# Kernel tuning notes

Measured on AMD Instinct MI355X. Metric: run time of the kernel, lower is better.

## Reference

```python
import jax, jax.numpy as jnp
import numpy as np

D_MODEL = 1024
HEADS = 16
D_KEY = D_MODEL // HEADS


def setup_inputs() -> dict:
    key = jax.random.key(0)
    ks = jax.random.split(key, 7)
    B, S = 4, 2048
    queries = jax.random.normal(ks[0], (B, S, D_MODEL), dtype=jnp.float32)
    keys = jax.random.normal(ks[1], (B, S, D_MODEL), dtype=jnp.float32)
    values = jax.random.normal(ks[2], (B, S, D_MODEL), dtype=jnp.float32)
    scale = 1.0 / np.sqrt(D_MODEL)
    # Per-head projection weights, torch Linear layout [out=d_key, in=d_model], stacked over heads
    Wq = jax.random.uniform(ks[3], (HEADS, D_KEY, D_MODEL), jnp.float32, -scale, scale)
    Wk = jax.random.uniform(ks[4], (HEADS, D_KEY, D_MODEL), jnp.float32, -scale, scale)
    Wv = jax.random.uniform(ks[5], (HEADS, D_KEY, D_MODEL), jnp.float32, -scale, scale)
    Wo = jax.random.uniform(ks[6], (D_MODEL, D_MODEL), jnp.float32, -scale, scale)
    return {"queries": queries, "keys": keys, "values": values,
            "Wq": Wq, "Wk": Wk, "Wv": Wv, "Wo": Wo}


def reference(queries, keys, values, Wq, Wk, Wv, Wo):
    # Project per head: [B,S,D] x [H,K,D] -> [B,H,S,K]
    q = jnp.einsum('bsd,hkd->bhsk', queries, Wq)
    k = jnp.einsum('bsd,hkd->bhsk', keys, Wk)
    v = jnp.einsum('bsd,hkd->bhsk', values, Wv)
    attn = jnp.einsum('bhqk,bhsk->bhqs', q, k) / jnp.sqrt(jnp.float32(D_KEY))
    attn = jax.nn.softmax(attn, axis=-1)
    out = jnp.einsum('bhqs,bhsk->bhqk', attn, v)  # [B,H,S,K]
    B, H, S, K = out.shape
    # concat heads along last dim (head order = torch cat order)
    out = out.transpose(0, 2, 1, 3).reshape(B, S, H * K)
    return out @ Wo.T
```

## Files before the change

kernel.cpp:

```cpp
#include <hip/hip_runtime.h>
#include <hip/hip_bf16.h>

typedef __attribute__((ext_vector_type(8))) short short8;
typedef __attribute__((ext_vector_type(4))) short short4v;
typedef __attribute__((ext_vector_type(4))) float f32x4;
typedef __bf16 bf16x8 __attribute__((ext_vector_type(8)));
typedef __attribute__((ext_vector_type(2))) unsigned int u32x2;
typedef __attribute__((ext_vector_type(4))) unsigned int u32x4;

#define DEVI static __device__ __forceinline__

DEVI short f2bs(float f) {
    union { __hip_bfloat16 h; short s; } u;
    u.h = __float2bfloat16(f);
    return u.s;
}

DEVI unsigned pack2(float a, float b) {
    union { short s[2]; unsigned u; } u;
    u.s[0] = f2bs(a);
    u.s[1] = f2bs(b);
    return u.u;
}

DEVI void xchg(unsigned& x, unsigned& y) {
#if __has_builtin(__builtin_amdgcn_permlane32_swap) && __has_builtin(__builtin_amdgcn_permlane16_swap)
    u32x2 t = __builtin_amdgcn_permlane32_swap(x, y, false, false);
    u32x2 r = __builtin_amdgcn_permlane16_swap(t[0], t[1], false, false);
    x = r[0];
    y = r[1];
#else
    asm("v_permlane32_swap_b32 %0, %1" : "+v"(x), "+v"(y));
    asm("v_permlane16_swap_b32 %0, %1" : "+v"(x), "+v"(y));
#endif
}

DEVI f32x4 mfma16(short8 a, short8 b, f32x4 c) {
    return __builtin_amdgcn_mfma_f32_16x16x32_bf16(
        __builtin_bit_cast(bf16x8, a), __builtin_bit_cast(bf16x8, b), c, 0, 0, 0);
}

DEVI void glds16(const short* g, short* l) {
    __builtin_amdgcn_global_load_lds((const __attribute__((address_space(1))) void*)g,
                                     (__attribute__((address_space(3))) void*)l, 16, 0, 0);
}

__global__ __launch_bounds__(256) void cvt_all(const float4* __restrict__ q,
                                               const float4* __restrict__ k,
                                               const float4* __restrict__ v,
                                               const float4* __restrict__ wq,
                                               const float4* __restrict__ wk,
                                               const float4* __restrict__ wv,
                                               const float4* __restrict__ wo,
                                               short4v* __restrict__ dq,
                                               short4v* __restrict__ dk,
                                               short4v* __restrict__ dv,
                                               short4v* __restrict__ dwq,
                                               short4v* __restrict__ dwk,
                                               short4v* __restrict__ dwv,
                                               short4v* __restrict__ dwo) {
    int bid = blockIdx.x;
    float4 x;
    short4v s;
    if (bid < 8192) {
        int i = bid * 256 + threadIdx.x;
        x = q[i]; s.x = f2bs(x.x); s.y = f2bs(x.y); s.z = f2bs(x.z); s.w = f2bs(x.w); dq[i] = s;
        x = k[i]; s.x = f2bs(x.x); s.y = f2bs(x.y); s.z = f2bs(x.z); s.w = f2bs(x.w); dk[i] = s;
        x = v[i]; s.x = f2bs(x.x); s.y = f2bs(x.y); s.z = f2bs(x.z); s.w = f2bs(x.w); dv[i] = s;
    } else {
        int i = (bid - 8192) * 256 + threadIdx.x;
        x = wq[i]; s.x = f2bs(x.x); s.y = f2bs(x.y); s.z = f2bs(x.z); s.w = f2bs(x.w); dwq[i] = s;
        x = wk[i]; s.x = f2bs(x.x); s.y = f2bs(x.y); s.z = f2bs(x.z); s.w = f2bs(x.w); dwk[i] = s;
        x = wv[i]; s.x = f2bs(x.x); s.y = f2bs(x.y); s.z = f2bs(x.z); s.w = f2bs(x.w); dwv[i] = s;
        x = wo[i]; s.x = f2bs(x.x); s.y = f2bs(x.y); s.z = f2bs(x.z); s.w = f2bs(x.w); dwo[i] = s;
    }
}

template <typename EpiT>
DEVI void gemm_body(const short* A, const short* Bw, short* smem, int m0, int n0, EpiT epi) {
    short* As = smem;
    short* Bs = smem + 8192;
    const int t = threadIdx.x;
    const int lane = t & 63, w = t >> 6;
    const int col = lane & 15, quad = lane >> 4;
    const int wm = (w & 1) * 64, wn = (w >> 1) * 64;

    f32x4 acc[4][4];
#pragma unroll
    for (int i = 0; i < 4; ++i)
#pragma unroll
        for (int j = 0; j < 4; ++j) acc[i][j] = (f32x4){0.f, 0.f, 0.f, 0.f};

    for (int kt = 0; kt < 16; ++kt) {
        const int k0 = kt * 64;
#pragma unroll
        for (int j = 0; j < 4; ++j) {
            int cbase = (j * 4 + w) * 64;
            int c = cbase + lane;
            int row = c >> 3, kc = (c & 7) ^ (row & 7);
            glds16(A + (size_t)(m0 + row) * 1024 + k0 + kc * 8, As + cbase * 8);
        }
#pragma unroll
        for (int j = 0; j < 4; ++j) {
            int cbase = (j * 4 + w) * 64;
            int c = cbase + lane;
            int row = c >> 3, kc = (c & 7) ^ (row & 7);
            glds16(Bw + (size_t)(n0 + row) * 1024 + k0 + kc * 8, Bs + cbase * 8);
        }
        __syncthreads();
#pragma unroll
        for (int ks = 0; ks < 2; ++ks) {
            short8 a[4], b[4];
#pragma unroll
            for (int i = 0; i < 4; ++i) {
                int row = wm + i * 16 + col;
                int kc = (ks * 4 + quad) ^ (col & 7);
                a[i] = *(const short8*)(As + (row * 8 + kc) * 8);
            }
#pragma unroll
            for (int i = 0; i < 4; ++i) {
                int row = wn + i * 16 + col;
                int kc = (ks * 4 + quad) ^ (col & 7);
                b[i] = *(const short8*)(Bs + (row * 8 + kc) * 8);
            }
#pragma unroll
            for (int mi = 0; mi < 4; ++mi)
#pragma unroll
                for (int ni = 0; ni < 4; ++ni)
                    acc[mi][ni] = mfma16(a[mi], b[ni], acc[mi][ni]);
        }
        __syncthreads();
    }
    epi(acc, wm, wn, col, quad);
}

__global__ __launch_bounds__(256) void qkv_gemm(const short* __restrict__ xq,
                                                const short* __restrict__ xk,
                                                const short* __restrict__ xv,
                                                const short* __restrict__ wq,
                                                const short* __restrict__ wk,
                                                const short* __restrict__ wv,
                                                short* __restrict__ qp,
                                                short* __restrict__ kp,
                                                short* __restrict__ vpt, float qscale) {
    __shared__ __align__(16) short smem[17408];
    const int z = blockIdx.z;
    const int m0 = blockIdx.y * 128, n0 = blockIdx.x * 128;
    const short* A = (z == 0) ? xq : (z == 1) ? xk : xv;
    const short* W = (z == 0) ? wq : (z == 1) ? wk : wv;

    if (z < 2) {
        short* outs = (z == 0) ? qp : kp;
        const float scale = (z == 0) ? qscale : 1.0f;
        gemm_body(A, W, smem, m0, n0, [&](f32x4 (&acc)[4][4], int wm, int wn, int col, int quad) {
            short* T = smem;
#pragma unroll
            for (int mi = 0; mi < 4; ++mi)
#pragma unroll
                for (int ni = 0; ni < 4; ++ni)
#pragma unroll
                    for (int r = 0; r < 4; ++r)
                        T[(wm + mi * 16 + quad * 4 + r) * 136 + wn + ni * 16 + col] =
                            f2bs(acc[mi][ni][r] * scale);
            __syncthreads();
            int t = threadIdx.x;
            int ml = t >> 1, nh = (t & 1) * 64;
            int m = m0 + ml;
            int b = m >> 11, s = m & 2047;
#pragma unroll
            for (int j = 0; j < 8; ++j) {
                int n = n0 + nh + j * 8;
                short8 vv = *(const short8*)(T + ml * 136 + nh + j * 8);
                size_t off = ((size_t)(b * 16 + (n >> 6)) * 2048 + s) * 64 + (n & 63);
                *(short8*)(outs + off) = vv;
            }
        });
    } else {
        gemm_body(A, W, smem, m0, n0, [&](f32x4 (&acc)[4][4], int wm, int wn, int col, int quad) {
            short* T = smem;
#pragma unroll
            for (int mi = 0; mi < 4; ++mi)
#pragma unroll
                for (int ni = 0; ni < 4; ++ni) {
                    int n_l = wn + ni * 16 + col;
                    int m_l = wm + mi * 16 + quad * 4;
                    short4v sv;
                    sv.x = f2bs(acc[mi][ni][0]); sv.y = f2bs(acc[mi][ni][1]);
                    sv.z = f2bs(acc[mi][ni][2]); sv.w = f2bs(acc[mi][ni][3]);
                    *(short4v*)(T + n_l * 132 + m_l) = sv;
                }
            __syncthreads();
            int t = threadIdx.x;
            int nrow = t >> 1, mh = (t & 1) * 64;
            int b = m0 >> 11, s0 = m0 & 2047;
            size_t base = ((size_t)(b * 1024 + n0 + nrow)) * 2048 + s0 + mh;
#pragma unroll
            for (int j = 0; j < 16; ++j) {
                unsigned long long vv = *(const unsigned long long*)(T + nrow * 132 + mh + j * 4);
                *(unsigned long long*)(vpt + base + j * 4) = vv;
            }
        });
    }
}

__global__ __launch_bounds__(256) void out_gemm(const short* __restrict__ ao,
                                                const short* __restrict__ wo,
                                                float* __restrict__ outf) {
    __shared__ __align__(16) short smem[16896];
    const int m0 = blockIdx.y * 128, n0 = blockIdx.x * 128;
    gemm_body(ao, wo, smem, m0, n0, [&](f32x4 (&acc)[4][4], int wm, int wn, int col, int quad) {
#pragma unroll
        for (int mi = 0; mi < 4; ++mi)
#pragma unroll
            for (int ni = 0; ni < 4; ++ni)
#pragma unroll
                for (int r = 0; r < 4; ++r) {
                    int m = m0 + wm + mi * 16 + quad * 4 + r;
                    int n = n0 + wn + ni * 16 + col;
                    outf[(size_t)m * 1024 + n] = acc[mi][ni][r];
                }
    });
}

__global__ __launch_bounds__(256, 4) void flash_attn(const short* __restrict__ qp,
                                                     const short* __restrict__ kp,
                                                     const short* __restrict__ vpt,
                                                     short* __restrict__ ao) {
    __shared__ __align__(16) short smem[16384];
    short* Ks2 = smem;
    short* Vs2 = smem + 8192;

    const int t = threadIdx.x, lane = t & 63, w = t >> 6;
    const int col = lane & 15, quad = lane >> 4;
    const int bh = blockIdx.x, q0 = blockIdx.y * 128;
    const short* qb = qp + (size_t)bh * 2048 * 64;
    const short* kb = kp + (size_t)bh * 2048 * 64;
    const short* vb = vpt + (size_t)bh * 64 * 2048;

#pragma unroll
    for (int j = 0; j < 4; ++j) {
        int cbase = (j * 4 + w) * 64;
        int c = cbase + lane;
        int row = c >> 3, kc = (c & 7) ^ (row & 7);
        glds16(qb + (size_t)(q0 + row) * 64 + kc * 8, smem + cbase * 8);
    }
    __syncthreads();
    short8 bQ[2][2];
#pragma unroll
    for (int qi = 0; qi < 2; ++qi)
#pragma unroll
        for (int ks = 0; ks < 2; ++ks) {
            int row = w * 32 + qi * 16 + col;
            int kc = (ks * 4 + quad) ^ (col & 7);
            bQ[qi][ks] = *(const short8*)(smem + (row * 8 + kc) * 8);
        }
    __syncthreads();

    const int base2_0 = col * 64 + ((quad ^ (col & 7)) * 8);
    const int base2_1 = col * 64 + (((4 + quad) ^ (col & 7)) * 8);

    const short* kg0;
    const short* kg1;
    const short* vg0;
    const short* vg1;
    {
        int c0 = w * 64 + lane, c1 = (4 + w) * 64 + lane;
        int r0 = c0 >> 3, p0 = c0 & 7, r1 = c1 >> 3, p1 = c1 & 7;
        kg0 = kb + r0 * 64 + ((p0 ^ (r0 & 7)) * 8);
        kg1 = kb + r1 * 64 + ((p1 ^ (r1 & 7)) * 8);
        vg0 = vb + (size_t)r0 * 2048 + ((p0 ^ (r0 & 7)) * 8);
        vg1 = vb + (size_t)r1 * 2048 + ((p1 ^ (r1 & 7)) * 8);
    }

    f32x4 acc_o[2][4], acc_l[2];
#pragma unroll
    for (int qi = 0; qi < 2; ++qi) {
        acc_l[qi] = (f32x4){0.f, 0.f, 0.f, 0.f};
#pragma unroll
        for (int ni = 0; ni < 4; ++ni) acc_o[qi][ni] = (f32x4){0.f, 0.f, 0.f, 0.f};
    }
    const short ONE = 0x3F80;
    const short8 vones = {ONE, ONE, ONE, ONE, ONE, ONE, ONE, ONE};

    glds16(kg0, Ks2 + w * 512);
    glds16(kg1, Ks2 + (4 + w) * 512);
    glds16(vg0, Vs2 + w * 512);
    glds16(vg1, Vs2 + (4 + w) * 512);
    kg0 += 4096; kg1 += 4096; vg0 += 64; vg1 += 64;
    __syncthreads();

#pragma unroll 2
    for (int kt = 0; kt < 32; ++kt) {
        const int cur = kt & 1;
        if (kt < 31) {
            const int nxt = cur ^ 1;
            glds16(kg0, Ks2 + nxt * 4096 + w * 512);
            glds16(kg1, Ks2 + nxt * 4096 + (4 + w) * 512);
            glds16(vg0, Vs2 + nxt * 4096 + w * 512);
            glds16(vg1, Vs2 + nxt * 4096 + (4 + w) * 512);
            kg0 += 4096; kg1 += 4096; vg0 += 64; vg1 += 64;
        }
        const short* Ks = Ks2 + cur * 4096;
        const short* Vs = Vs2 + cur * 4096;

#pragma unroll
        for (int g = 0; g < 2; ++g) {
            unsigned pdw[2][4];
#pragma unroll
            for (int h = 0; h < 2; ++h) {
                const int kei = g * 2 + h;
                f32x4 st0 = (f32x4){0.f, 0.f, 0.f, 0.f};
                f32x4 st1 = (f32x4){0.f, 0.f, 0.f, 0.f};
                __builtin_amdgcn_s_setprio(1);
                {
                    short8 aK0 = *(const short8*)(Ks + base2_0 + kei * 1024);
                    st0 = mfma16(aK0, bQ[0][0], st0);
                    st1 = mfma16(aK0, bQ[1][0], st1);
                    short8 aK1 = *(const short8*)(Ks + base2_1 + kei * 1024);
                    st0 = mfma16(aK1, bQ[0][1], st0);
                    st1 = mfma16(aK1, bQ[1][1], st1);
                }
                __builtin_amdgcn_s_setprio(0);
                {
                    float p0 = __builtin_amdgcn_exp2f(st0[0]);
                    float p1 = __builtin_amdgcn_exp2f(st0[1]);
                    float p2 = __builtin_amdgcn_exp2f(st0[2]);
                    float p3 = __builtin_amdgcn_exp2f(st0[3]);
                    pdw[0][h * 2] = pack2(p0, p1);
                    pdw[0][h * 2 + 1] = pack2(p2, p3);
                }
                {
                    float p0 = __builtin_amdgcn_exp2f(st1[0]);
                    float p1 = __builtin_amdgcn_exp2f(st1[1]);
                    float p2 = __builtin_amdgcn_exp2f(st1[2]);
                    float p3 = __builtin_amdgcn_exp2f(st1[3]);
                    pdw[1][h * 2] = pack2(p0, p1);
                    pdw[1][h * 2 + 1] = pack2(p2, p3);
                }
            }
            xchg(pdw[0][0], pdw[0][2]);
            xchg(pdw[0][1], pdw[0][3]);
            xchg(pdw[1][0], pdw[1][2]);
            xchg(pdw[1][1], pdw[1][3]);
            u32x4 pv0 = {pdw[0][0], pdw[0][1], pdw[0][2], pdw[0][3]};
            u32x4 pv1 = {pdw[1][0], pdw[1][1], pdw[1][2], pdw[1][3]};
            short8 pa0 = __builtin_bit_cast(short8, pv0);
            short8 pa1 = __builtin_bit_cast(short8, pv1);

            const int vb2 = (g == 0) ? base2_0 : base2_1;
            __builtin_amdgcn_s_setprio(1);
#pragma unroll
            for (int ni = 0; ni < 4; ++ni) {
                short8 bv = *(const short8*)(Vs + vb2 + ni * 1024);
                acc_o[0][ni] = mfma16(pa0, bv, acc_o[0][ni]);
                acc_o[1][ni] = mfma16(pa1, bv, acc_o[1][ni]);
            }
            acc_l[0] = mfma16(pa0, vones, acc_l[0]);
            acc_l[1] = mfma16(pa1, vones, acc_l[1]);
            __builtin_amdgcn_s_setprio(0);
        }
        __syncthreads();
    }

    const int b = bh >> 4, hd = bh & 15;
#pragma unroll
    for (int qi = 0; qi < 2; ++qi)
#pragma unroll
        for (int r = 0; r < 4; ++r) {
            float inv = 1.0f / acc_l[qi][r];
            int q = q0 + w * 32 + qi * 16 + quad * 4 + r;
#pragma unroll
            for (int ni = 0; ni < 4; ++ni)
                ao[((size_t)(b * 2048 + q)) * 1024 + hd * 64 + ni * 16 + col] =
                    f2bs(acc_o[qi][ni][r] * inv);
        }
}

extern "C" void kernel_launch(void* const* d_in, const int* in_sizes, int n_in,
                              void* d_out, int out_size, void* d_ws, size_t ws_size,
                              hipStream_t stream) {
    const float* q  = (const float*)d_in[0];
    const float* k  = (const float*)d_in[1];
    const float* v  = (const float*)d_in[2];
    const float* Wq = (const float*)d_in[3];
    const float* Wk = (const float*)d_in[4];
    const float* Wv = (const float*)d_in[5];
    const float* Wo = (const float*)d_in[6];
    float* out = (float*)d_out;

    short* ws = (short*)d_ws;
    const size_t SZ = (size_t)64 * 2048 * 64;
    const size_t WZ = (size_t)1024 * 1024;
    short* xq  = ws;
    short* xk  = ws + SZ;
    short* xv  = ws + 2 * SZ;
    short* qp  = ws + 3 * SZ;
    short* kp  = ws + 4 * SZ;
    short* wqb = ws + 5 * SZ;
    short* wkb = wqb + WZ;
    short* wvb = wqb + 2 * WZ;
    short* wob = wqb + 3 * WZ;
    short* ao  = xq;
    short* vpt = xk;

    const float QSCALE = 0.125f * 1.44269504088896f;

    cvt_all<<<dim3(9216), dim3(256), 0, stream>>>(
        (const float4*)q, (const float4*)k, (const float4*)v, (const float4*)Wq,
        (const float4*)Wk, (const float4*)Wv, (const float4*)Wo, (short4v*)xq, (short4v*)xk,
        (short4v*)xv, (short4v*)wqb, (short4v*)wkb, (short4v*)wvb, (short4v*)wob);
    dim3 blk(256);
    qkv_gemm<<<dim3(8, 64, 3), blk, 0, stream>>>(xq, xk, xv, wqb, wkb, wvb, qp, kp, vpt, QSCALE);
    flash_attn<<<dim3(64, 16), blk, 0, stream>>>(qp, kp, vpt, ao);
    out_gemm<<<dim3(8, 64), blk, 0, stream>>>(ao, wob, out);
}
```

Measured before the change: 338.7 us.

## Double-buffer GEMM K-loop with 32-wide tiles and XCD-aware block remapping

The shared GEMM body now uses a double-buffered LDS pipeline with 32-wide K tiles: the next tile's global-to-LDS loads are issued before the current tile's MFMAs, removing one barrier per iteration. The LDS layout and swizzle are reworked, pointers are precomputed, and MFMA sections are wrapped in s_setprio. The QKV and output GEMM grids remap block IDs so consecutive blocks spread across the chiplets (XCDs). The transposed V buffer moves into the output buffer, so it no longer aliases the key input workspace. Each k-step carries less work, which risks more per-iteration overhead, and the new swizzle must stay bank-conflict free.

```diff
diff --git a/kernel.cpp b/kernel.cpp
--- a/kernel.cpp
+++ b/kernel.cpp
@@ -78,57 +78,67 @@
 
 template <typename EpiT>
 DEVI void gemm_body(const short* A, const short* Bw, short* smem, int m0, int n0, EpiT epi) {
-    short* As = smem;
-    short* Bs = smem + 8192;
     const int t = threadIdx.x;
     const int lane = t & 63, w = t >> 6;
     const int col = lane & 15, quad = lane >> 4;
     const int wm = (w & 1) * 64, wn = (w >> 1) * 64;
 
+    const short* pA0;
+    const short* pA1;
+    const short* pB0;
+    const short* pB1;
+    {
+        int i0 = w * 64 + lane, i1 = (4 + w) * 64 + lane;
+        int L0 = i0 >> 3, cc0 = (i0 & 7) ^ (L0 & 7);
+        int r0 = 2 * L0 + (cc0 & 1), c0 = cc0 >> 1;
+        int L1 = i1 >> 3, cc1 = (i1 & 7) ^ (L1 & 7);
+        int r1 = 2 * L1 + (cc1 & 1), c1 = cc1 >> 1;
+        pA0 = A + (size_t)(m0 + r0) * 1024 + c0 * 8;
+        pA1 = A + (size_t)(m0 + r1) * 1024 + c1 * 8;
+        pB0 = Bw + (size_t)(n0 + r0) * 1024 + c0 * 8;
+        pB1 = Bw + (size_t)(n0 + r1) * 1024 + c1 * 8;
+    }
+    const int posa = (2 * quad + (col & 1)) ^ (col >> 1);
+    const int base_a = wm * 32 + (col >> 1) * 64 + posa * 8;
+    const int base_b = wn * 32 + (col >> 1) * 64 + posa * 8;
+
     f32x4 acc[4][4];
 #pragma unroll
     for (int i = 0; i < 4; ++i)
 #pragma unroll
         for (int j = 0; j < 4; ++j) acc[i][j] = (f32x4){0.f, 0.f, 0.f, 0.f};
 
-    for (int kt = 0; kt < 16; ++kt) {
-        const int k0 = kt * 64;
-#pragma unroll
-        for (int j = 0; j < 4; ++j) {
-            int cbase = (j * 4 + w) * 64;
-            int c = cbase + lane;
-            int row = c >> 3, kc = (c & 7) ^ (row & 7);
-            glds16(A + (size_t)(m0 + row) * 1024 + k0 + kc * 8, As + cbase * 8);
+    glds16(pA0, smem + w * 512);
+    glds16(pA1, smem + (4 + w) * 512);
+    glds16(pB0, smem + 4096 + w * 512);
+    glds16(pB1, smem + 4096 + (4 + w) * 512);
+    pA0 += 32; pA1 += 32; pB0 += 32; pB1 += 32;
+    __syncthreads();
+
+#pragma unroll 2
+    for (int kt = 0; kt < 32; ++kt) {
+        const int cur = kt & 1;
+        const short* Cb = smem + cur * 8192;
+        if (kt < 31) {
+            short* Nb = smem + (cur ^ 1) * 8192;
+            glds16(pA0, Nb + w * 512);
+            glds16(pA1, Nb + (4 + w) * 512);
+            glds16(pB0, Nb + 4096 + w * 512);
+            glds16(pB1, Nb + 4096 + (4 + w) * 512);
+            pA0 += 32; pA1 += 32; pB0 += 32; pB1 += 32;
         }
-#pragma unroll
-        for (int j = 0; j < 4; ++j) {
-            int cbase = (j * 4 + w) * 64;
-            int c = cbase + lane;
-            int row = c >> 3, kc = (c & 7) ^ (row & 7);
-            glds16(Bw + (size_t)(n0 + row) * 1024 + k0 + kc * 8, Bs + cbase * 8);
-        }
-        __syncthreads();
-#pragma unroll
-        for (int ks = 0; ks < 2; ++ks) {
-            short8 a[4], b[4];
-#pragma unroll
-            for (int i = 0; i < 4; ++i) {
-                int row = wm + i * 16 + col;
-                int kc = (ks * 4 + quad) ^ (col & 7);
-                a[i] = *(const short8*)(As + (row * 8 + kc) * 8);
-            }
-#pragma unroll
-            for (int i = 0; i < 4; ++i) {
-                int row = wn + i * 16 + col;
-                int kc = (ks * 4 + quad) ^ (col & 7);
-                b[i] = *(const short8*)(Bs + (row * 8 + kc) * 8);
-            }
-#pragma unroll
-            for (int mi = 0; mi < 4; ++mi)
-#pragma unroll
-                for (int ni = 0; ni < 4; ++ni)
-                    acc[mi][ni] = mfma16(a[mi], b[ni], acc[mi][ni]);
-        }
+        short8 a[4], b[4];
+#pragma unroll
+        for (int i = 0; i < 4; ++i) a[i] = *(const short8*)(Cb + base_a + i * 512);
+#pragma unroll
+        for (int i = 0; i < 4; ++i) b[i] = *(const short8*)(Cb + 4096 + base_b + i * 512);
+        __builtin_amdgcn_s_setprio(1);
+#pragma unroll
+        for (int mi = 0; mi < 4; ++mi)
+#pragma unroll
+            for (int ni = 0; ni < 4; ++ni)
+                acc[mi][ni] = mfma16(a[mi], b[ni], acc[mi][ni]);
+        __builtin_amdgcn_s_setprio(0);
         __syncthreads();
     }
     epi(acc, wm, wn, col, quad);
@@ -144,8 +154,11 @@
                                                 short* __restrict__ kp,
                                                 short* __restrict__ vpt, float qscale) {
     __shared__ __align__(16) short smem[17408];
-    const int z = blockIdx.z;
-    const int m0 = blockIdx.y * 128, n0 = blockIdx.x * 128;
+    const int lin = blockIdx.x + (blockIdx.y << 3) + (blockIdx.z << 9);
+    const int wgid = (lin & 7) * 192 + (lin >> 3);
+    const int n0 = (wgid & 7) * 128;
+    const int m0 = ((wgid >> 3) & 63) * 128;
+    const int z = wgid >> 9;
     const short* A = (z == 0) ? xq : (z == 1) ? xk : xv;
     const short* W = (z == 0) ? wq : (z == 1) ? wk : wv;
 
@@ -207,7 +220,10 @@
                                                 const short* __restrict__ wo,
                                                 float* __restrict__ outf) {
     __shared__ __align__(16) short smem[16896];
-    const int m0 = blockIdx.y * 128, n0 = blockIdx.x * 128;
+    const int lin = blockIdx.x + (blockIdx.y << 3);
+    const int wgid = (lin & 7) * 64 + (lin >> 3);
+    const int n0 = (wgid & 7) * 128;
+    const int m0 = (wgid >> 3) * 128;
     gemm_body(ao, wo, smem, m0, n0, [&](f32x4 (&acc)[4][4], int wm, int wn, int col, int quad) {
 #pragma unroll
         for (int mi = 0; mi < 4; ++mi)
@@ -401,7 +417,7 @@
     short* wvb = wqb + 2 * WZ;
     short* wob = wqb + 3 * WZ;
     short* ao  = xq;
-    short* vpt = xk;
+    short* vpt = (short*)d_out;
 
     const float QSCALE = 0.125f * 1.44269504088896f;
 
```

Measured after the change: 331.0 us, median of 2. 2.3% less time.
